# Performance work log

Measured on AMD Instinct MI355X. Metric: run time of the kernel, lower is better.

## Reference

```python
import jax, jax.numpy as jnp
import numpy as np

B, P, T = 32, 196, 32           # batch, num pixels (14*14), seq_len
E, H, A, V = 512, 512, 256, 30000  # embed, hidden, attention, vocab
FEAT = 2048

def _ln(x, g, b, eps=1e-5):
    m = jnp.mean(x, -1, keepdims=True)
    v = jnp.mean((x - m) ** 2, -1, keepdims=True)
    return (x - m) / jnp.sqrt(v + eps) * g + b

def setup_inputs() -> dict:
    key = jax.random.key(0)
    ks = iter(jax.random.split(key, 32))
    def rn(shape, s=0.05):
        return (jax.random.normal(next(ks), shape, dtype=jnp.float32) * s)
    inp = {
        'features': jax.random.normal(next(ks), (B, P, FEAT), dtype=jnp.float32),
        'captions': jax.random.randint(next(ks), (B, T), 0, V),
        # feature adapter Linear(2048->E) + LayerNorm
        'Wad': rn((E, FEAT)), 'bad': jnp.zeros((E,), jnp.float32),
        'g_ad': jnp.ones((E,), jnp.float32), 'b_ad': jnp.zeros((E,), jnp.float32),
        # additive attention
        'We': rn((A, E)), 'be': jnp.zeros((A,), jnp.float32),
        'Wd': rn((A, H)), 'bd': jnp.zeros((A,), jnp.float32),
        'Wf': rn((1, A)), 'bf': jnp.zeros((1,), jnp.float32),
        # embedding table (uniform(-0.1,0.1) as in torch init)
        'emb': jax.random.uniform(next(ks), (V, E), jnp.float32, -0.1, 0.1),
        # LSTM layer 0: input 2E, layer 1: input H; gates order i,f,g,o; forget bias 1
        'W_ih0': rn((4 * H, 2 * E)), 'W_hh0': rn((4 * H, H)),
        'b_ih0': jnp.concatenate([jnp.zeros(H), jnp.ones(H), jnp.zeros(2 * H)]).astype(jnp.float32),
        'b_hh0': jnp.zeros((4 * H,), jnp.float32),
        'W_ih1': rn((4 * H, H)), 'W_hh1': rn((4 * H, H)),
        'b_ih1': jnp.concatenate([jnp.zeros(H), jnp.ones(H), jnp.zeros(2 * H)]).astype(jnp.float32),
        'b_hh1': jnp.zeros((4 * H,), jnp.float32),
        # output head
        'W1': rn((H // 2, H)), 'b1': jnp.zeros((H // 2,), jnp.float32),
        'g1': jnp.ones((H // 2,), jnp.float32), 'bb1': jnp.zeros((H // 2,), jnp.float32),
        'W2': rn((V, H // 2)), 'b2': jnp.zeros((V,), jnp.float32),
    }
    return inp

def reference(features, captions, Wad, bad, g_ad, b_ad, We, be, Wd, bd, Wf, bf,
              emb, W_ih0, W_hh0, b_ih0, b_hh0, W_ih1, W_hh1, b_ih1, b_hh1,
              W1, b1, g1, bb1, W2, b2):
    # feature adapter (dropout = identity in eval)
    enc = _ln(jax.nn.relu(features @ Wad.T + bad), g_ad, b_ad)   # [B,P,E]
    att1 = enc @ We.T + be                                        # [B,P,A] (same every step)
    embs = emb[captions]                                          # [B,T,E]

    def lstm_cell(x, h, c, Wih, Whh, bih, bhh):
        gates = x @ Wih.T + bih + h @ Whh.T + bhh                 # [B,4H]
        i, f, g, o = jnp.split(gates, 4, axis=1)
        c_n = jax.nn.sigmoid(f) * c + jax.nn.sigmoid(i) * jnp.tanh(g)
        h_n = jax.nn.sigmoid(o) * jnp.tanh(c_n)
        return h_n, c_n

    def step(carry, emb_t):
        h, c = carry                                              # each [2,B,H]
        # additive attention against top-layer hidden state
        att2 = h[1] @ Wd.T + bd                                   # [B,A]
        e = (jax.nn.relu(att1 + att2[:, None, :]) @ Wf.T + bf)[..., 0]  # [B,P]
        alpha = jax.nn.softmax(e, axis=1)                         # (max-subtract is folded in)
        ctx = jnp.einsum('bp,bpe->be', alpha, enc)                # [B,E]
        x = jnp.concatenate([emb_t, ctx], axis=1)                 # [B,2E]
        h0, c0 = lstm_cell(x,  h[0], c[0], W_ih0, W_hh0, b_ih0, b_hh0)
        h1, c1 = lstm_cell(h0, h[1], c[1], W_ih1, W_hh1, b_ih1, b_hh1)
        out = jax.nn.relu(_ln(h1 @ W1.T + b1, g1, bb1))
        out = jnp.clip(out @ W2.T + b2, -10.0, 10.0)              # [B,V]
        return (jnp.stack([h0, h1]), jnp.stack([c0, c1])), out

    h0 = jnp.zeros((2, B, H), jnp.float32)
    c0 = jnp.zeros((2, B, H), jnp.float32)
    _, outs = jax.lax.scan(step, (h0, c0), jnp.swapaxes(embs, 0, 1))
    return jnp.swapaxes(outs, 0, 1)                               # [B,T,V]
```

## Files before the change

kernel.cpp:

```cpp
#include <hip/hip_runtime.h>

#define B_ 32
#define P_ 196
#define T_ 32
#define E_ 512
#define H_ 512
#define A_ 256
#define V_ 30000
#define FEAT_ 2048

typedef unsigned short u16;
typedef __attribute__((ext_vector_type(8))) short bf16x8;
typedef __attribute__((ext_vector_type(4))) float fx4;

#define MFMA16 __builtin_amdgcn_mfma_f32_16x16x32_bf16

__device__ __forceinline__ u16 f2b(float f){
  unsigned u = __builtin_bit_cast(unsigned, f);
  u += 0x7FFFu + ((u >> 16) & 1u);
  return (u16)(u >> 16);
}
__device__ __forceinline__ float b2f(u16 h){
  unsigned u = ((unsigned)h) << 16;
  return __builtin_bit_cast(float, u);
}
__device__ __forceinline__ float sigm(float x){ return 1.f/(1.f + __expf(-x)); }

__global__ void k_convert(const float* __restrict__ src, u16* __restrict__ dst, int n8){
  int i = blockIdx.x*256 + threadIdx.x;
  if (i >= n8) return;
  const float4* s = (const float4*)src + (size_t)i*2;
  float4 a = s[0], b = s[1];
  ushort4* d = (ushort4*)dst + (size_t)i*2;
  d[0] = make_ushort4(f2b(a.x), f2b(a.y), f2b(a.z), f2b(a.w));
  d[1] = make_ushort4(f2b(b.x), f2b(b.y), f2b(b.z), f2b(b.w));
}

__global__ void k_gather(const float* __restrict__ emb, const int* __restrict__ cap,
                         u16* __restrict__ dst){
  int r = blockIdx.x, l = threadIdx.x;
  int t = r >> 5, b = r & 31;
  int c = cap[b*T_ + t];
  const float4* s = (const float4*)(emb + (size_t)c*E_) + l*2;
  float4 a = s[0], bb = s[1];
  ushort4* d = (ushort4*)(dst + (size_t)r*E_) + l*2;
  d[0] = make_ushort4(f2b(a.x), f2b(a.y), f2b(a.z), f2b(a.w));
  d[1] = make_ushort4(f2b(bb.x), f2b(bb.y), f2b(bb.z), f2b(bb.w));
}

__global__ void k_pack_wd2(const float* __restrict__ Wd, unsigned* __restrict__ dst){
  int i = blockIdx.x*256 + threadIdx.x;
  if (i >= 256*256) return;
  int n = i & 255, kp = i >> 8;
  unsigned lo = f2b(Wd[n*512 + 2*kp]);
  unsigned hi = f2b(Wd[n*512 + 2*kp + 1]);
  dst[i] = lo | (hi << 16);
}

__global__ void k_pack_g0(const float* __restrict__ Wih, const float* __restrict__ Whh,
                          u16* __restrict__ dst){
  int eid = blockIdx.x*256 + threadIdx.x;
  if (eid >= 6144*512) return;
  int j = eid & 7, l = (eid >> 3) & 63, frag = eid >> 9;
  int ks = frag % 12; int rest = frag / 12;
  int kw = rest & 3, q = (rest >> 2) & 3, s = rest >> 4;
  int n = q*512 + s*16 + (l & 15);
  int k = kw*384 + ks*32 + ((l >> 4) << 3) + j;
  float v = (k < 1024) ? Wih[(size_t)n*1024 + k] : Whh[(size_t)n*512 + (k - 1024)];
  dst[eid] = f2b(v);
}

__global__ void k_pack_w1p(const float* __restrict__ Wih, const float* __restrict__ Whh,
                           u16* __restrict__ dst){
  int eid = blockIdx.x*256 + threadIdx.x;
  if (eid >= 32*128*512) return;
  int j = eid & 7, l = (eid >> 3) & 63, f = eid >> 9;
  int nf = f & 127, s = f >> 7;
  int np = nf*16 + (l & 15);
  int k = ((l >> 4) << 3) + j;
  int orig = ((np >> 4) & 3)*512 + (np >> 6)*16 + (np & 15);
  float v = (k < 16) ? Wih[(size_t)orig*512 + s*16 + k]
                     : Whh[(size_t)orig*512 + s*16 + (k - 16)];
  dst[eid] = f2b(v);
}

__global__ void k_bias_pack(const float* __restrict__ bih, const float* __restrict__ bhh,
                            float* __restrict__ dst){
  int n = blockIdx.x*256 + threadIdx.x;
  if (n >= 2048) return;
  int c = n & 15, q = (n >> 4) & 3, s = n >> 6;
  int orig = q*512 + s*16 + c;
  dst[n] = bih[orig] + bhh[orig];
}

template<int MODE, int BM, int BN>
__launch_bounds__(256)
__global__ void k_gemm(const u16* __restrict__ A, const u16* __restrict__ W,
                       const float* __restrict__ bias, float* __restrict__ outF,
                       u16* __restrict__ outB, int M, int N, int K){
  constexpr int NI = BN/32, MI = BM/32;
  __shared__ __align__(16) u16 As[BM][40];
  __shared__ __align__(16) u16 Bs[BN][40];
  int tid = threadIdx.x;
  int l = tid & 63, w = tid >> 6;
  int wr = w >> 1, wc = w & 1;
  int m0 = blockIdx.y * BM, n0 = blockIdx.x * BN;
  fx4 acc[MI][NI];
  #pragma unroll
  for (int i=0;i<MI;i++)
    #pragma unroll
    for (int j=0;j<NI;j++) acc[i][j] = (fx4){0.f,0.f,0.f,0.f};
  int r = tid >> 2, seg = tid & 3;
  int lr = l & 15, lg = l >> 4;
  for (int k0 = 0; k0 < K; k0 += 32){
    #pragma unroll
    for (int pa=0; pa<BM/64; pa++)
      *(uint4*)&As[r+pa*64][seg*8] = *(const uint4*)(A + (size_t)(m0+r+pa*64)*K + k0 + seg*8);
    uint4 z = {0u,0u,0u,0u};
    #pragma unroll
    for (int pb=0; pb<BN/64; pb++){
      int rb = n0 + r + pb*64;
      *(uint4*)&Bs[r+pb*64][seg*8] = (rb < N) ? *(const uint4*)(W + (size_t)rb*K + k0 + seg*8) : z;
    }
    __syncthreads();
    bf16x8 av[MI], bv[NI];
    #pragma unroll
    for (int mi=0; mi<MI; mi++) av[mi] = *(const bf16x8*)&As[wr*(BM/2) + mi*16 + lr][lg*8];
    #pragma unroll
    for (int ni=0; ni<NI; ni++) bv[ni] = *(const bf16x8*)&Bs[wc*(BN/2) + ni*16 + lr][lg*8];
    #pragma unroll
    for (int mi=0; mi<MI; mi++)
      #pragma unroll
      for (int ni=0; ni<NI; ni++)
        acc[mi][ni] = MFMA16(av[mi], bv[ni], acc[mi][ni], 0, 0, 0);
    __syncthreads();
  }
  #pragma unroll
  for (int mi=0; mi<MI; mi++)
    #pragma unroll
    for (int ni=0; ni<NI; ni++){
      int col = n0 + wc*(BN/2) + ni*16 + lr;
      if (col >= N) continue;
      float bvs = bias[col];
      #pragma unroll
      for (int reg=0; reg<4; reg++){
        int rowm = m0 + wr*(BM/2) + mi*16 + lg*4 + reg;
        float v = acc[mi][ni][reg] + bvs;
        if (MODE == 0){ v = fmaxf(v, 0.f); outB[(size_t)rowm*N + col] = f2b(v); }
        else if (MODE == 1){ outB[(size_t)rowm*N + col] = f2b(v); }
        else if (MODE == 2){ outF[(size_t)rowm*N + col] = v; }
        else {
          v = fminf(fmaxf(v, -10.f), 10.f);
          outF[(size_t)rowm*V_ + col] = v;
        }
      }
    }
}

__global__ void k_ln1(const u16* __restrict__ pre, const float* __restrict__ g,
                      const float* __restrict__ bt, u16* __restrict__ enc){
  int row = blockIdx.x; int l = threadIdx.x;
  bf16x8 vv = *(const bf16x8*)(pre + (size_t)row*E_ + l*8);
  float x[8]; float s = 0.f;
  #pragma unroll
  for (int i=0;i<8;i++){ x[i] = b2f((u16)vv[i]); s += x[i]; }
  #pragma unroll
  for (int off=32; off; off>>=1) s += __shfl_xor(s, off, 64);
  float mean = s * (1.f/512.f);
  float vs = 0.f;
  #pragma unroll
  for (int i=0;i<8;i++){ float d = x[i]-mean; vs += d*d; }
  #pragma unroll
  for (int off=32; off; off>>=1) vs += __shfl_xor(vs, off, 64);
  float inv = rsqrtf(vs*(1.f/512.f) + 1e-5f);
  int c0 = l*8;
  u16 o[8];
  #pragma unroll
  for (int i=0;i<8;i++) o[i] = f2b((x[i]-mean)*inv*g[c0+i] + bt[c0+i]);
  ushort4* d = (ushort4*)(enc + (size_t)row*E_ + c0);
  d[0] = make_ushort4(o[0],o[1],o[2],o[3]);
  d[1] = make_ushort4(o[4],o[5],o[6],o[7]);
}

__global__ void k_ln2(const float* __restrict__ pre1, const float* __restrict__ g,
                      const float* __restrict__ bb, u16* __restrict__ hid){
  int row = blockIdx.x; int l = threadIdx.x;
  float4 v = *(const float4*)(pre1 + (size_t)row*256 + l*4);
  float x[4] = {v.x, v.y, v.z, v.w};
  float s = x[0]+x[1]+x[2]+x[3];
  #pragma unroll
  for (int off=32; off; off>>=1) s += __shfl_xor(s, off, 64);
  float mean = s * (1.f/256.f);
  float vs = 0.f;
  #pragma unroll
  for (int i=0;i<4;i++){ float d = x[i]-mean; vs += d*d; }
  #pragma unroll
  for (int off=32; off; off>>=1) vs += __shfl_xor(vs, off, 64);
  float inv = rsqrtf(vs*(1.f/256.f) + 1e-5f);
  int c0 = l*4;
  u16 o[4];
  #pragma unroll
  for (int i=0;i<4;i++) o[i] = f2b(fmaxf((x[i]-mean)*inv*g[c0+i] + bb[c0+i], 0.f));
  *(ushort4*)(hid + (size_t)row*256 + c0) = make_ushort4(o[0],o[1],o[2],o[3]);
}

__launch_bounds__(1024)
__global__ void k_ly(const float* __restrict__ part1, const float* __restrict__ bias1p,
                     float* __restrict__ c1buf, u16* __restrict__ h1all,
                     const unsigned* __restrict__ Wd2, const float* __restrict__ bd,
                     const u16* __restrict__ att1b, const u16* __restrict__ enc16,
                     const float* __restrict__ Wf, const float* __restrict__ bfp,
                     const u16* __restrict__ embs, u16* __restrict__ xh0cur, int t){
  int b = blockIdx.x, tid = threadIdx.x;
  int l = tid & 63, wid = tid >> 6;
  __shared__ float g1s[2048];
  __shared__ float h1s[512];
  __shared__ float a2p[4][256];
  __shared__ float a2[256], ev[256], red[8], wfv[256], bdv[256];
  __shared__ float cb[4][256][2];
  if (tid < 256){ wfv[tid] = Wf[tid]; bdv[tid] = bd[tid]; }
  float bf0 = bfp[0];

  if (t > 0){
    float acc0 = bias1p[tid], acc1 = bias1p[tid + 1024];
    #pragma unroll 4
    for (int s2=0; s2<32; ++s2){
      const float* pp = part1 + ((size_t)(s2*32 + b))*2048;
      acc0 += pp[tid];
      acc1 += pp[tid + 1024];
    }
    g1s[tid] = acc0; g1s[tid + 1024] = acc1;
    __syncthreads();
    if (tid < 512){
      int h = tid, s4 = h >> 4, c = h & 15, base = s4*64 + c;
      float gi = g1s[base], gf = g1s[base+16], gg = g1s[base+32], go = g1s[base+48];
      float cold = c1buf[b*512 + h];
      float cn = sigm(gf)*cold + sigm(gi)*tanhf(gg);
      c1buf[b*512 + h] = cn;
      float hn = sigm(go)*tanhf(cn);
      h1s[h] = hn;
      h1all[((size_t)b*T_ + (t-1))*512 + h] = f2b(hn);
    }
  } else {
    if (tid < 512) h1s[tid] = 0.f;
  }
  __syncthreads();
  if (t >= T_) return;

  {
    int n = tid & 255, kq = tid >> 8;
    float acc = 0.f;
    const unsigned* wp = Wd2 + (size_t)kq*64*256 + n;
    #pragma unroll 8
    for (int kp2 = 0; kp2 < 64; ++kp2){
      unsigned wv = wp[(size_t)kp2*256];
      int k0 = (kq*64 + kp2)*2;
      acc += h1s[k0]   * b2f((u16)(wv & 0xFFFFu))
           + h1s[k0+1] * b2f((u16)(wv >> 16));
    }
    a2p[kq][n] = acc;
  }
  __syncthreads();
  if (tid < 256) a2[tid] = a2p[0][tid] + a2p[1][tid] + a2p[2][tid] + a2p[3][tid] + bdv[tid];
  __syncthreads();
  for (int pi = 0; pi < 13; ++pi){
    int p = pi*16 + wid;
    if (p < P_){
      ushort4 av4 = *(const ushort4*)(att1b + (size_t)(b*P_ + p)*A_ + l*4);
      int j0 = l*4;
      float sum = fmaxf(b2f(av4.x)+a2[j0],  0.f)*wfv[j0]
                + fmaxf(b2f(av4.y)+a2[j0+1],0.f)*wfv[j0+1]
                + fmaxf(b2f(av4.z)+a2[j0+2],0.f)*wfv[j0+2]
                + fmaxf(b2f(av4.w)+a2[j0+3],0.f)*wfv[j0+3];
      #pragma unroll
      for (int off=32; off; off>>=1) sum += __shfl_xor(sum, off, 64);
      if (l == 0) ev[p] = sum + bf0;
    }
  }
  __syncthreads();
  if (tid < 256){
    float v = (tid < P_) ? ev[tid] : -1e30f;
    float m = v;
    #pragma unroll
    for (int off=32; off; off>>=1) m = fmaxf(m, __shfl_xor(m, off, 64));
    if (l == 0) red[wid] = m;
  }
  __syncthreads();
  float mg = fmaxf(fmaxf(red[0],red[1]), fmaxf(red[2],red[3]));
  if (tid < 256){
    float ex = (tid < P_) ? __expf(ev[tid] - mg) : 0.f;
    float ss = ex;
    #pragma unroll
    for (int off=32; off; off>>=1) ss += __shfl_xor(ss, off, 64);
    if (l == 0) red[4+wid] = ss;
    ev[tid] = ex;
  }
  __syncthreads();
  float inv = 1.f/(red[4]+red[5]+red[6]+red[7]);
  {
    int j = tid & 255, pq = tid >> 8;
    float A0 = 0.f, A1 = 0.f;
    const unsigned* ep = (const unsigned*)enc16 + ((size_t)b*P_ + pq*49)*256 + j;
    #pragma unroll 7
    for (int pi = 0; pi < 49; ++pi){
      unsigned vv = ep[(size_t)pi*256];
      float al = ev[pq*49 + pi];
      A0 += al * b2f((u16)(vv & 0xFFFFu));
      A1 += al * b2f((u16)(vv >> 16));
    }
    cb[pq][j][0] = A0; cb[pq][j][1] = A1;
  }
  __syncthreads();
  if (tid < 256){
    float c0 = (cb[0][tid][0]+cb[1][tid][0]+cb[2][tid][0]+cb[3][tid][0]) * inv;
    float c1 = (cb[0][tid][1]+cb[1][tid][1]+cb[2][tid][1]+cb[3][tid][1]) * inv;
    unsigned o = (unsigned)f2b(c0) | (((unsigned)f2b(c1)) << 16);
    *((unsigned*)(xh0cur + (size_t)b*1536 + 512) + tid) = o;
    ((unsigned*)(xh0cur + (size_t)b*1536))[tid] =
        ((const unsigned*)(embs + (size_t)(t*32+b)*E_))[tid];
  }
}

__launch_bounds__(1024)
__global__ void k_lx(const u16* __restrict__ xh0cur, u16* __restrict__ xh0nxt,
                     const u16* __restrict__ Wg0pk, const float* __restrict__ bias0p,
                     const u16* __restrict__ W1ppk, const u16* __restrict__ h1all,
                     float* __restrict__ c0buf, float* __restrict__ part1, int t){
  __shared__ float part[16][32][16];
  __shared__ float gsum[4][32][16];
  __shared__ __align__(16) u16 As[32][40];
  int tid = threadIdx.x, s = blockIdx.x;
  int l = tid & 63, kw = tid >> 6, lr = l & 15, lg = l >> 4;

  bf16x8 a[2][3];
  #pragma unroll
  for (int mi=0;mi<2;mi++)
    #pragma unroll
    for (int ks=0;ks<3;ks++)
      a[mi][ks] = *(const bf16x8*)(xh0cur + (size_t)(mi*16+lr)*1536 + kw*96 + ks*32 + lg*8);
  for (int q=0;q<4;q++){
    fx4 acc0 = (fx4){0,0,0,0}, acc1 = (fx4){0,0,0,0};
    const u16* wp = Wg0pk + (size_t)(((s*4+q)*4 + (kw>>2))*12 + (kw&3)*3)*512 + l*8;
    #pragma unroll
    for (int ks=0;ks<3;ks++){
      bf16x8 bf8 = *(const bf16x8*)(wp + ks*512);
      acc0 = MFMA16(a[0][ks], bf8, acc0, 0,0,0);
      acc1 = MFMA16(a[1][ks], bf8, acc1, 0,0,0);
    }
    #pragma unroll
    for (int reg=0;reg<4;reg++){
      part[kw][lg*4+reg][lr]    = acc0[reg];
      part[kw][16+lg*4+reg][lr] = acc1[reg];
    }
    __syncthreads();
    if (tid < 512){
      int bb = tid >> 4, c = tid & 15;
      float g = bias0p[s*64 + q*16 + c];
      #pragma unroll
      for (int kw2=0; kw2<16; ++kw2) g += part[kw2][bb][c];
      gsum[q][bb][c] = g;
    }
    __syncthreads();
  }
  if (tid < 256){
    int bb = tid >> 3, kk = (tid & 7)*2;
    unsigned hv = 0;
    if (t > 0) hv = *(const unsigned*)(h1all + ((size_t)bb*T_ + (t-1))*512 + s*16 + kk);
    *(unsigned*)&As[bb][16+kk] = hv;
  }
  if (tid < 512){
    int bb = tid >> 4, c = tid & 15;
    int h = s*16 + c;
    float gi = gsum[0][bb][c], gf = gsum[1][bb][c], gg = gsum[2][bb][c], go = gsum[3][bb][c];
    float cold = c0buf[bb*512 + h];
    float cn = sigm(gf)*cold + sigm(gi)*tanhf(gg);
    c0buf[bb*512 + h] = cn;
    u16 hb = f2b(sigm(go)*tanhf(cn));
    xh0nxt[(size_t)bb*1536 + 1024 + h] = hb;
    As[bb][c] = hb;
  }
  __syncthreads();
  bf16x8 pa0 = *(const bf16x8*)&As[lr][lg*8];
  bf16x8 pa1 = *(const bf16x8*)&As[16+lr][lg*8];
  #pragma unroll 2
  for (int i=0;i<8;i++){
    int nf = kw*8 + i;
    bf16x8 bf8 = *(const bf16x8*)(W1ppk + (size_t)(s*128 + nf)*512 + l*8);
    fx4 A0 = MFMA16(pa0, bf8, (fx4){0,0,0,0}, 0,0,0);
    fx4 A1 = MFMA16(pa1, bf8, (fx4){0,0,0,0}, 0,0,0);
    float* o = part1 + ((size_t)s*32)*2048 + nf*16 + lr;
    #pragma unroll
    for (int reg=0;reg<4;reg++){
      o[(size_t)(lg*4+reg)*2048]    = A0[reg];
      o[(size_t)(16+lg*4+reg)*2048] = A1[reg];
    }
  }
}

extern "C" void kernel_launch(void* const* d_in, const int* in_sizes, int n_in,
                              void* d_out, int out_size, void* d_ws, size_t ws_size,
                              hipStream_t stream){
  (void)in_sizes; (void)n_in; (void)out_size; (void)ws_size;
  const float* features = (const float*)d_in[0];
  const int*   captions = (const int*)d_in[1];
  const float* Wad  = (const float*)d_in[2];
  const float* bad  = (const float*)d_in[3];
  const float* g_ad = (const float*)d_in[4];
  const float* b_ad = (const float*)d_in[5];
  const float* We   = (const float*)d_in[6];
  const float* be   = (const float*)d_in[7];
  const float* Wd   = (const float*)d_in[8];
  const float* bd   = (const float*)d_in[9];
  const float* Wf   = (const float*)d_in[10];
  const float* bfp  = (const float*)d_in[11];
  const float* emb  = (const float*)d_in[12];
  const float* W_ih0 = (const float*)d_in[13];
  const float* W_hh0 = (const float*)d_in[14];
  const float* b_ih0 = (const float*)d_in[15];
  const float* b_hh0 = (const float*)d_in[16];
  const float* W_ih1 = (const float*)d_in[17];
  const float* W_hh1 = (const float*)d_in[18];
  const float* b_ih1 = (const float*)d_in[19];
  const float* b_hh1 = (const float*)d_in[20];
  const float* W1  = (const float*)d_in[21];
  const float* b1  = (const float*)d_in[22];
  const float* g1  = (const float*)d_in[23];
  const float* bb1 = (const float*)d_in[24];
  const float* W2  = (const float*)d_in[25];
  const float* b2  = (const float*)d_in[26];
  float* out = (float*)d_out;

  char* wsb = (char*)d_ws;
  size_t off = 0;
  auto alloc = [&](size_t bytes)->char*{
    char* p = wsb + off; off += (bytes + 255) & ~(size_t)255; return p;
  };
  u16* fb16    = (u16*)alloc((size_t)6272*2048*2);
  u16* Wad16   = (u16*)alloc((size_t)512*2048*2);
  u16* We16    = (u16*)alloc((size_t)256*512*2);
  u16* W1_16   = (u16*)alloc((size_t)256*512*2);
  u16* W2_16   = (u16*)alloc((size_t)30000*256*2);
  unsigned* Wd2 = (unsigned*)alloc((size_t)256*256*4);
  u16* Wg0pk   = (u16*)alloc((size_t)2048*1536*2);
  u16* W1ppk   = (u16*)alloc((size_t)32*128*512*2);
  float* bias0p = (float*)alloc(2048*4);
  float* bias1p = (float*)alloc(2048*4);
  u16* embs16  = (u16*)alloc((size_t)1024*512*2);
  u16* pre16   = (u16*)alloc((size_t)6272*512*2);
  u16* enc16   = (u16*)alloc((size_t)6272*512*2);
  u16* att1_16 = (u16*)alloc((size_t)6272*256*2);
  u16* xh0     = (u16*)alloc((size_t)2*32*1536*2);
  float* c0buf = (float*)alloc(32*512*4);
  float* c1buf = (float*)alloc(32*512*4);
  float* part1 = (float*)alloc((size_t)32*32*2048*4);
  u16* h1all16 = (u16*)alloc((size_t)1024*512*2);
  float* pre1  = (float*)alloc((size_t)1024*256*4);
  u16* hid16   = (u16*)alloc((size_t)1024*256*2);

  auto cdiv = [](int a, int b){ return (a+b-1)/b; };

  hipMemsetAsync(xh0, 0, 196608 + 65536 + 65536, stream);

  k_convert<<<cdiv(6272*2048/8,256),256,0,stream>>>(features, fb16, 6272*2048/8);
  k_convert<<<cdiv(512*2048/8,256),256,0,stream>>>(Wad, Wad16, 512*2048/8);
  k_convert<<<cdiv(256*512/8,256),256,0,stream>>>(We, We16, 256*512/8);
  k_convert<<<cdiv(256*512/8,256),256,0,stream>>>(W1, W1_16, 256*512/8);
  k_convert<<<cdiv(30000*256/8,256),256,0,stream>>>(W2, W2_16, 30000*256/8);
  k_pack_wd2<<<cdiv(256*256,256),256,0,stream>>>(Wd, Wd2);
  k_pack_g0<<<cdiv(6144*512,256),256,0,stream>>>(W_ih0, W_hh0, Wg0pk);
  k_pack_w1p<<<cdiv(32*128*512,256),256,0,stream>>>(W_ih1, W_hh1, W1ppk);
  k_bias_pack<<<8,256,0,stream>>>(b_ih0, b_hh0, bias0p);
  k_bias_pack<<<8,256,0,stream>>>(b_ih1, b_hh1, bias1p);
  k_gather<<<1024,64,0,stream>>>(emb, captions, embs16);

  k_gemm<0,64,64><<<dim3(8,98),256,0,stream>>>(fb16, Wad16, bad, nullptr, pre16, 6272, 512, 2048);
  k_ln1<<<6272,64,0,stream>>>(pre16, g_ad, b_ad, enc16);
  k_gemm<1,64,64><<<dim3(4,98),256,0,stream>>>(enc16, We16, be, nullptr, att1_16, 6272, 256, 512);

  u16* xb[2] = { xh0, xh0 + 32*1536 };
  for (int t = 0; t < T_; ++t){
    k_ly<<<32,1024,0,stream>>>(part1, bias1p, c1buf, h1all16, Wd2, bd,
                               att1_16, enc16, Wf, bfp, embs16, xb[t&1], t);
    k_lx<<<32,1024,0,stream>>>(xb[t&1], xb[1-(t&1)], Wg0pk, bias0p,
                               W1ppk, h1all16, c0buf, part1, t);
  }
  k_ly<<<32,1024,0,stream>>>(part1, bias1p, c1buf, h1all16, Wd2, bd,
                             att1_16, enc16, Wf, bfp, embs16, xb[0], T_);

  k_gemm<2,64,64><<<dim3(4,16),256,0,stream>>>(h1all16, W1_16, b1, pre1, nullptr, 1024, 256, 512);
  k_ln2<<<1024,64,0,stream>>>(pre1, g1, bb1, hid16);
  k_gemm<3,64,128><<<dim3(235,16),256,0,stream>>>(hid16, W2_16, b2, out, nullptr, 1024, 30000, 256);
}
```

Before: 1.395 ms.

## Overlap output head and W2 conversion with recurrent steps on idle CUs

The recurrent kernels only use 32 blocks, leaving most CUs idle. Extra blocks are added to each step launch. For the first steps they convert W2 to bf16, and afterwards they compute the W1+LayerNorm projection and the vocab head for the previous timestep. This hides the large head GEMM behind the serial recurrence and removes the separate tail GEMMs. The cost is more blocks per launch, a larger shared footprint, and finer-grained head tiles that reload W2 every step.

New measurement: 1.653 ms. +18.5%, slower.

```diff
diff --git a/kernel.cpp b/kernel.cpp
--- a/kernel.cpp
+++ b/kernel.cpp
@@ -25,6 +25,17 @@
   return __builtin_bit_cast(float, u);
 }
 __device__ __forceinline__ float sigm(float x){ return 1.f/(1.f + __expf(-x)); }
+
+struct RecLyS {
+  float g1s[2048]; float h1s[512]; float a2p[4][256];
+  float a2[256]; float ev[256]; float red[8]; float wfv[256]; float bdv[256];
+  float cb[4][256][2];
+};
+struct RecLxS {
+  float part[16][32][16]; float gsum[4][32][16]; u16 As[32][40];
+};
+struct HeadS { u16 hA[32][264]; u16 hB[256][40]; };
+struct W1S   { float red2[1024]; float mv[64]; };
 
 __global__ void k_convert(const float* __restrict__ src, u16* __restrict__ dst, int n8){
   int i = blockIdx.x*256 + threadIdx.x;
@@ -96,8 +107,8 @@
 template<int MODE, int BM, int BN>
 __launch_bounds__(256)
 __global__ void k_gemm(const u16* __restrict__ A, const u16* __restrict__ W,
-                       const float* __restrict__ bias, float* __restrict__ outF,
-                       u16* __restrict__ outB, int M, int N, int K){
+                       const float* __restrict__ bias, u16* __restrict__ outB,
+                       int M, int N, int K){
   constexpr int NI = BN/32, MI = BM/32;
   __shared__ __align__(16) u16 As[BM][40];
   __shared__ __align__(16) u16 Bs[BN][40];
@@ -146,13 +157,8 @@
       for (int reg=0; reg<4; reg++){
         int rowm = m0 + wr*(BM/2) + mi*16 + lg*4 + reg;
         float v = acc[mi][ni][reg] + bvs;
-        if (MODE == 0){ v = fmaxf(v, 0.f); outB[(size_t)rowm*N + col] = f2b(v); }
-        else if (MODE == 1){ outB[(size_t)rowm*N + col] = f2b(v); }
-        else if (MODE == 2){ outF[(size_t)rowm*N + col] = v; }
-        else {
-          v = fminf(fmaxf(v, -10.f), 10.f);
-          outF[(size_t)rowm*V_ + col] = v;
-        }
+        if (MODE == 0) v = fmaxf(v, 0.f);
+        outB[(size_t)rowm*N + col] = f2b(v);
       }
     }
 }
@@ -182,26 +188,115 @@
   d[1] = make_ushort4(o[4],o[5],o[6],o[7]);
 }
 
-__global__ void k_ln2(const float* __restrict__ pre1, const float* __restrict__ g,
-                      const float* __restrict__ bb, u16* __restrict__ hid){
-  int row = blockIdx.x; int l = threadIdx.x;
-  float4 v = *(const float4*)(pre1 + (size_t)row*256 + l*4);
-  float x[4] = {v.x, v.y, v.z, v.w};
-  float s = x[0]+x[1]+x[2]+x[3];
-  #pragma unroll
-  for (int off=32; off; off>>=1) s += __shfl_xor(s, off, 64);
-  float mean = s * (1.f/256.f);
-  float vs = 0.f;
-  #pragma unroll
-  for (int i=0;i<4;i++){ float d = x[i]-mean; vs += d*d; }
-  #pragma unroll
-  for (int off=32; off; off>>=1) vs += __shfl_xor(vs, off, 64);
-  float inv = rsqrtf(vs*(1.f/256.f) + 1e-5f);
-  int c0 = l*4;
-  u16 o[4];
-  #pragma unroll
-  for (int i=0;i<4;i++) o[i] = f2b(fmaxf((x[i]-mean)*inv*g[c0+i] + bb[c0+i], 0.f));
-  *(ushort4*)(hid + (size_t)row*256 + c0) = make_ushort4(o[0],o[1],o[2],o[3]);
+__device__ __forceinline__ void w2cvt_chunk(const float* __restrict__ W2f,
+                                            u16* __restrict__ W2b, int cw, int tid){
+  int i = cw*1024 + tid;
+  if (i >= (V_*A_)/8) return;
+  const float4* s = (const float4*)W2f + (size_t)i*2;
+  float4 a = s[0], b = s[1];
+  ushort4* d = (ushort4*)W2b + (size_t)i*2;
+  d[0] = make_ushort4(f2b(a.x), f2b(a.y), f2b(a.z), f2b(a.w));
+  d[1] = make_ushort4(f2b(b.x), f2b(b.y), f2b(b.z), f2b(b.w));
+}
+
+__device__ __forceinline__ void w1ln_block(const u16* __restrict__ h1all,
+    const u16* __restrict__ W1, const float* __restrict__ b1,
+    const float* __restrict__ g1v, const float* __restrict__ bb1,
+    u16* __restrict__ hid, int u, int tid, float* red2, float* mv){
+  int l = tid & 63, w = tid >> 6, lr = l & 15, lg = l >> 4;
+  fx4 acc[2] = {{0,0,0,0},{0,0,0,0}};
+  for (int k0 = 0; k0 < 512; k0 += 32){
+    bf16x8 bv  = *(const bf16x8*)(W1 + (size_t)(w*16+lr)*512 + k0 + lg*8);
+    bf16x8 av0 = *(const bf16x8*)(h1all + ((size_t)lr*T_ + u)*512 + k0 + lg*8);
+    bf16x8 av1 = *(const bf16x8*)(h1all + ((size_t)(16+lr)*T_ + u)*512 + k0 + lg*8);
+    acc[0] = MFMA16(av0, bv, acc[0], 0,0,0);
+    acc[1] = MFMA16(av1, bv, acc[1], 0,0,0);
+  }
+  int col = w*16 + lr;
+  float bc = b1[col];
+  float val[2][4], s1[2][4], s2[2][4];
+  #pragma unroll
+  for (int mi=0;mi<2;mi++)
+    #pragma unroll
+    for (int reg=0;reg<4;reg++){
+      float v = acc[mi][reg] + bc;
+      val[mi][reg] = v; s1[mi][reg] = v; s2[mi][reg] = v*v;
+    }
+  #pragma unroll
+  for (int off=1; off<16; off<<=1){
+    #pragma unroll
+    for (int mi=0;mi<2;mi++)
+      #pragma unroll
+      for (int reg=0;reg<4;reg++){
+        s1[mi][reg] += __shfl_xor(s1[mi][reg], off, 64);
+        s2[mi][reg] += __shfl_xor(s2[mi][reg], off, 64);
+      }
+  }
+  if (lr == 0){
+    #pragma unroll
+    for (int mi=0;mi<2;mi++)
+      #pragma unroll
+      for (int reg=0;reg<4;reg++){
+        int row = mi*16 + lg*4 + reg;
+        red2[(0*16 + w)*32 + row] = s1[mi][reg];
+        red2[(16   + w)*32 + row] = s2[mi][reg];
+      }
+  }
+  __syncthreads();
+  if (tid < 64){
+    int which = tid >> 5, row = tid & 31;
+    float s = 0.f;
+    #pragma unroll
+    for (int ww=0; ww<16; ++ww) s += red2[(which*16 + ww)*32 + row];
+    mv[which*32 + row] = s;
+  }
+  __syncthreads();
+  #pragma unroll
+  for (int mi=0;mi<2;mi++)
+    #pragma unroll
+    for (int reg=0;reg<4;reg++){
+      int row = mi*16 + lg*4 + reg;
+      float mean = mv[row] * (1.f/256.f);
+      float var  = mv[32+row] * (1.f/256.f) - mean*mean;
+      float inv  = rsqrtf(var + 1e-5f);
+      float o = fmaxf((val[mi][reg]-mean)*inv*g1v[col] + bb1[col], 0.f);
+      hid[((size_t)u*32 + row)*256 + col] = f2b(o);
+    }
+}
+
+__device__ __forceinline__ void head_chunk(const u16* __restrict__ hid,
+    const u16* __restrict__ W2, const float* __restrict__ b2,
+    float* __restrict__ out, int u, int c, int tid,
+    u16 (*hA)[264], u16 (*hB)[40]){
+  if (c >= 118) return;
+  int l = tid & 63, w = tid >> 6, lr = l & 15, lg = l >> 4;
+  int v0 = c*256;
+  { int arow = tid >> 5, ak = (tid & 31)*8;
+    *(uint4*)&hA[arow][ak] = *(const uint4*)(hid + ((size_t)u*32 + arow)*256 + ak); }
+  fx4 acc0 = {0,0,0,0}, acc1 = {0,0,0,0};
+  int r = tid >> 2, seg = tid & 3;
+  for (int k0 = 0; k0 < 256; k0 += 32){
+    uint4 z = {0u,0u,0u,0u};
+    int rb = v0 + r;
+    *(uint4*)&hB[r][seg*8] = (rb < V_) ? *(const uint4*)(W2 + (size_t)rb*256 + k0 + seg*8) : z;
+    __syncthreads();
+    bf16x8 bv  = *(const bf16x8*)&hB[w*16 + lr][lg*8];
+    bf16x8 av0 = *(const bf16x8*)&hA[lr][k0 + lg*8];
+    bf16x8 av1 = *(const bf16x8*)&hA[16 + lr][k0 + lg*8];
+    acc0 = MFMA16(av0, bv, acc0, 0,0,0);
+    acc1 = MFMA16(av1, bv, acc1, 0,0,0);
+    __syncthreads();
+  }
+  int col = v0 + w*16 + lr;
+  if (col < V_){
+    float bb = b2[col];
+    #pragma unroll
+    for (int reg=0; reg<4; reg++){
+      int r0 = lg*4 + reg, r1 = 16 + lg*4 + reg;
+      out[((size_t)r0*T_ + u)*V_ + col] = fminf(fmaxf(acc0[reg]+bb, -10.f), 10.f);
+      out[((size_t)r1*T_ + u)*V_ + col] = fminf(fmaxf(acc1[reg]+bb, -10.f), 10.f);
+    }
+  }
 }
 
 __launch_bounds__(1024)
@@ -210,15 +305,27 @@
                      const unsigned* __restrict__ Wd2, const float* __restrict__ bd,
                      const u16* __restrict__ att1b, const u16* __restrict__ enc16,
                      const float* __restrict__ Wf, const float* __restrict__ bfp,
-                     const u16* __restrict__ embs, u16* __restrict__ xh0cur, int t){
-  int b = blockIdx.x, tid = threadIdx.x;
+                     const u16* __restrict__ embs, u16* __restrict__ xh0cur, int t,
+                     int auxmode, int auxp,
+                     const float* __restrict__ W2f, u16* __restrict__ W2b,
+                     const u16* __restrict__ hid16, const float* __restrict__ b2,
+                     float* __restrict__ out){
+  constexpr unsigned SB = sizeof(RecLyS) > sizeof(HeadS) ? sizeof(RecLyS) : sizeof(HeadS);
+  __shared__ __align__(16) char shbuf[SB];
+  int bid = blockIdx.x, tid = threadIdx.x;
+  if (bid >= 32){
+    int a = bid - 32;
+    if (auxmode == 1) w2cvt_chunk(W2f, W2b, auxp + a, tid);
+    else {
+      HeadS& HS = *(HeadS*)shbuf;
+      head_chunk(hid16, W2b, b2, out, auxp, a, tid, HS.hA, HS.hB);
+    }
+    return;
+  }
+  RecLyS& S = *(RecLyS*)shbuf;
+  int b = bid;
   int l = tid & 63, wid = tid >> 6;
-  __shared__ float g1s[2048];
-  __shared__ float h1s[512];
-  __shared__ float a2p[4][256];
-  __shared__ float a2[256], ev[256], red[8], wfv[256], bdv[256];
-  __shared__ float cb[4][256][2];
-  if (tid < 256){ wfv[tid] = Wf[tid]; bdv[tid] = bd[tid]; }
+  if (tid < 256){ S.wfv[tid] = Wf[tid]; S.bdv[tid] = bd[tid]; }
   float bf0 = bfp[0];
 
   if (t > 0){
@@ -229,20 +336,20 @@
       acc0 += pp[tid];
       acc1 += pp[tid + 1024];
     }
-    g1s[tid] = acc0; g1s[tid + 1024] = acc1;
+    S.g1s[tid] = acc0; S.g1s[tid + 1024] = acc1;
     __syncthreads();
     if (tid < 512){
       int h = tid, s4 = h >> 4, c = h & 15, base = s4*64 + c;
-      float gi = g1s[base], gf = g1s[base+16], gg = g1s[base+32], go = g1s[base+48];
+      float gi = S.g1s[base], gf = S.g1s[base+16], gg = S.g1s[base+32], go = S.g1s[base+48];
       float cold = c1buf[b*512 + h];
       float cn = sigm(gf)*cold + sigm(gi)*tanhf(gg);
       c1buf[b*512 + h] = cn;
       float hn = sigm(go)*tanhf(cn);
-      h1s[h] = hn;
+      S.h1s[h] = hn;
       h1all[((size_t)b*T_ + (t-1))*512 + h] = f2b(hn);
     }
   } else {
-    if (tid < 512) h1s[tid] = 0.f;
+    if (tid < 512) S.h1s[tid] = 0.f;
   }
   __syncthreads();
   if (t >= T_) return;
@@ -255,48 +362,48 @@
     for (int kp2 = 0; kp2 < 64; ++kp2){
       unsigned wv = wp[(size_t)kp2*256];
       int k0 = (kq*64 + kp2)*2;
-      acc += h1s[k0]   * b2f((u16)(wv & 0xFFFFu))
-           + h1s[k0+1] * b2f((u16)(wv >> 16));
-    }
-    a2p[kq][n] = acc;
-  }
-  __syncthreads();
-  if (tid < 256) a2[tid] = a2p[0][tid] + a2p[1][tid] + a2p[2][tid] + a2p[3][tid] + bdv[tid];
+      acc += S.h1s[k0]   * b2f((u16)(wv & 0xFFFFu))
+           + S.h1s[k0+1] * b2f((u16)(wv >> 16));
+    }
+    S.a2p[kq][n] = acc;
+  }
+  __syncthreads();
+  if (tid < 256) S.a2[tid] = S.a2p[0][tid] + S.a2p[1][tid] + S.a2p[2][tid] + S.a2p[3][tid] + S.bdv[tid];
   __syncthreads();
   for (int pi = 0; pi < 13; ++pi){
     int p = pi*16 + wid;
     if (p < P_){
       ushort4 av4 = *(const ushort4*)(att1b + (size_t)(b*P_ + p)*A_ + l*4);
       int j0 = l*4;
-      float sum = fmaxf(b2f(av4.x)+a2[j0],  0.f)*wfv[j0]
-                + fmaxf(b2f(av4.y)+a2[j0+1],0.f)*wfv[j0+1]
-                + fmaxf(b2f(av4.z)+a2[j0+2],0.f)*wfv[j0+2]
-                + fmaxf(b2f(av4.w)+a2[j0+3],0.f)*wfv[j0+3];
+      float sum = fmaxf(b2f(av4.x)+S.a2[j0],  0.f)*S.wfv[j0]
+                + fmaxf(b2f(av4.y)+S.a2[j0+1],0.f)*S.wfv[j0+1]
+                + fmaxf(b2f(av4.z)+S.a2[j0+2],0.f)*S.wfv[j0+2]
+                + fmaxf(b2f(av4.w)+S.a2[j0+3],0.f)*S.wfv[j0+3];
       #pragma unroll
       for (int off=32; off; off>>=1) sum += __shfl_xor(sum, off, 64);
-      if (l == 0) ev[p] = sum + bf0;
+      if (l == 0) S.ev[p] = sum + bf0;
     }
   }
   __syncthreads();
   if (tid < 256){
-    float v = (tid < P_) ? ev[tid] : -1e30f;
+    float v = (tid < P_) ? S.ev[tid] : -1e30f;
     float m = v;
     #pragma unroll
     for (int off=32; off; off>>=1) m = fmaxf(m, __shfl_xor(m, off, 64));
-    if (l == 0) red[wid] = m;
-  }
-  __syncthreads();
-  float mg = fmaxf(fmaxf(red[0],red[1]), fmaxf(red[2],red[3]));
+    if (l == 0) S.red[wid] = m;
+  }
+  __syncthreads();
+  float mg = fmaxf(fmaxf(S.red[0],S.red[1]), fmaxf(S.red[2],S.red[3]));
   if (tid < 256){
-    float ex = (tid < P_) ? __expf(ev[tid] - mg) : 0.f;
+    float ex = (tid < P_) ? __expf(S.ev[tid] - mg) : 0.f;
     float ss = ex;
     #pragma unroll
     for (int off=32; off; off>>=1) ss += __shfl_xor(ss, off, 64);
-    if (l == 0) red[4+wid] = ss;
-    ev[tid] = ex;
-  }
-  __syncthreads();
-  float inv = 1.f/(red[4]+red[5]+red[6]+red[7]);
+    if (l == 0) S.red[4+wid] = ss;
+    S.ev[tid] = ex;
+  }
+  __syncthreads();
+  float inv = 1.f/(S.red[4]+S.red[5]+S.red[6]+S.red[7]);
   {
     int j = tid & 255, pq = tid >> 8;
     float A0 = 0.f, A1 = 0.f;
@@ -304,16 +411,16 @@
     #pragma unroll 7
     for (int pi = 0; pi < 49; ++pi){
       unsigned vv = ep[(size_t)pi*256];
-      float al = ev[pq*49 + pi];
+      float al = S.ev[pq*49 + pi];
       A0 += al * b2f((u16)(vv & 0xFFFFu));
       A1 += al * b2f((u16)(vv >> 16));
     }
-    cb[pq][j][0] = A0; cb[pq][j][1] = A1;
+    S.cb[pq][j][0] = A0; S.cb[pq][j][1] = A1;
   }
   __syncthreads();
   if (tid < 256){
-    float c0 = (cb[0][tid][0]+cb[1][tid][0]+cb[2][tid][0]+cb[3][tid][0]) * inv;
-    float c1 = (cb[0][tid][1]+cb[1][tid][1]+cb[2][tid][1]+cb[3][tid][1]) * inv;
+    float c0 = (S.cb[0][tid][0]+S.cb[1][tid][0]+S.cb[2][tid][0]+S.cb[3][tid][0]) * inv;
+    float c1 = (S.cb[0][tid][1]+S.cb[1][tid][1]+S.cb[2][tid][1]+S.cb[3][tid][1]) * inv;
     unsigned o = (unsigned)f2b(c0) | (((unsigned)f2b(c1)) << 16);
     *((unsigned*)(xh0cur + (size_t)b*1536 + 512) + tid) = o;
     ((unsigned*)(xh0cur + (size_t)b*1536))[tid] =
@@ -325,11 +432,35 @@
 __global__ void k_lx(const u16* __restrict__ xh0cur, u16* __restrict__ xh0nxt,
                      const u16* __restrict__ Wg0pk, const float* __restrict__ bias0p,
                      const u16* __restrict__ W1ppk, const u16* __restrict__ h1all,
-                     float* __restrict__ c0buf, float* __restrict__ part1, int t){
-  __shared__ float part[16][32][16];
-  __shared__ float gsum[4][32][16];
-  __shared__ __align__(16) u16 As[32][40];
-  int tid = threadIdx.x, s = blockIdx.x;
+                     float* __restrict__ c0buf, float* __restrict__ part1, int t,
+                     int auxmode, int auxp,
+                     const float* __restrict__ W2f, u16* __restrict__ W2b,
+                     u16* __restrict__ hid16, const float* __restrict__ b2,
+                     float* __restrict__ out,
+                     const u16* __restrict__ W1_16, const float* __restrict__ b1,
+                     const float* __restrict__ g1v, const float* __restrict__ bb1){
+  constexpr unsigned SA = sizeof(RecLxS) > sizeof(HeadS) ? sizeof(RecLxS) : sizeof(HeadS);
+  constexpr unsigned SB = SA > sizeof(W1S) ? SA : sizeof(W1S);
+  __shared__ __align__(16) char shbuf[SB];
+  int bid = blockIdx.x, tid = threadIdx.x;
+  if (bid == 32){
+    if (t >= 1){
+      W1S& WS = *(W1S*)shbuf;
+      w1ln_block(h1all, W1_16, b1, g1v, bb1, hid16, t-1, tid, WS.red2, WS.mv);
+    }
+    return;
+  }
+  if (bid > 32){
+    int a = bid - 33;
+    if (auxmode == 1) w2cvt_chunk(W2f, W2b, auxp + a, tid);
+    else {
+      HeadS& HS = *(HeadS*)shbuf;
+      head_chunk(hid16, W2b, b2, out, auxp, 59 + a, tid, HS.hA, HS.hB);
+    }
+    return;
+  }
+  RecLxS& S = *(RecLxS*)shbuf;
+  int s = bid;
   int l = tid & 63, kw = tid >> 6, lr = l & 15, lg = l >> 4;
 
   bf16x8 a[2][3];
@@ -349,16 +480,16 @@
     }
     #pragma unroll
     for (int reg=0;reg<4;reg++){
-      part[kw][lg*4+reg][lr]    = acc0[reg];
-      part[kw][16+lg*4+reg][lr] = acc1[reg];
+      S.part[kw][lg*4+reg][lr]    = acc0[reg];
+      S.part[kw][16+lg*4+reg][lr] = acc1[reg];
     }
     __syncthreads();
     if (tid < 512){
       int bb = tid >> 4, c = tid & 15;
       float g = bias0p[s*64 + q*16 + c];
       #pragma unroll
-      for (int kw2=0; kw2<16; ++kw2) g += part[kw2][bb][c];
-      gsum[q][bb][c] = g;
+      for (int kw2=0; kw2<16; ++kw2) g += S.part[kw2][bb][c];
+      S.gsum[q][bb][c] = g;
     }
     __syncthreads();
   }
@@ -366,22 +497,22 @@
     int bb = tid >> 3, kk = (tid & 7)*2;
     unsigned hv = 0;
     if (t > 0) hv = *(const unsigned*)(h1all + ((size_t)bb*T_ + (t-1))*512 + s*16 + kk);
-    *(unsigned*)&As[bb][16+kk] = hv;
+    *(unsigned*)&S.As[bb][16+kk] = hv;
   }
   if (tid < 512){
     int bb = tid >> 4, c = tid & 15;
     int h = s*16 + c;
-    float gi = gsum[0][bb][c], gf = gsum[1][bb][c], gg = gsum[2][bb][c], go = gsum[3][bb][c];
+    float gi = S.gsum[0][bb][c], gf = S.gsum[1][bb][c], gg = S.gsum[2][bb][c], go = S.gsum[3][bb][c];
     float cold = c0buf[bb*512 + h];
     float cn = sigm(gf)*cold + sigm(gi)*tanhf(gg);
     c0buf[bb*512 + h] = cn;
     u16 hb = f2b(sigm(go)*tanhf(cn));
     xh0nxt[(size_t)bb*1536 + 1024 + h] = hb;
-    As[bb][c] = hb;
-  }
-  __syncthreads();
-  bf16x8 pa0 = *(const bf16x8*)&As[lr][lg*8];
-  bf16x8 pa1 = *(const bf16x8*)&As[16+lr][lg*8];
+    S.As[bb][c] = hb;
+  }
+  __syncthreads();
+  bf16x8 pa0 = *(const bf16x8*)&S.As[lr][lg*8];
+  bf16x8 pa1 = *(const bf16x8*)&S.As[16+lr][lg*8];
   #pragma unroll 2
   for (int i=0;i<8;i++){
     int nf = kw*8 + i;
@@ -395,6 +526,25 @@
       o[(size_t)(16+lg*4+reg)*2048] = A1[reg];
     }
   }
+}
+
+__launch_bounds__(1024)
+__global__ void k_aux(int w1t, int u, int cofs,
+                      const u16* __restrict__ h1all, const u16* __restrict__ W1_16,
+                      const float* __restrict__ b1, const float* __restrict__ g1v,
+                      const float* __restrict__ bb1, u16* __restrict__ hid16,
+                      const u16* __restrict__ W2b, const float* __restrict__ b2,
+                      float* __restrict__ out){
+  constexpr unsigned SB = sizeof(HeadS) > sizeof(W1S) ? sizeof(HeadS) : sizeof(W1S);
+  __shared__ __align__(16) char shbuf[SB];
+  int bid = blockIdx.x, tid = threadIdx.x;
+  if (bid == 0 && w1t >= 0){
+    W1S& WS = *(W1S*)shbuf;
+    w1ln_block(h1all, W1_16, b1, g1v, bb1, hid16, w1t, tid, WS.red2, WS.mv);
+    return;
+  }
+  HeadS& HS = *(HeadS*)shbuf;
+  head_chunk(hid16, W2b, b2, out, u, cofs + bid, tid, HS.hA, HS.hB);
 }
 
 extern "C" void kernel_launch(void* const* d_in, const int* in_sizes, int n_in,
@@ -454,7 +604,6 @@
   float* c1buf = (float*)alloc(32*512*4);
   float* part1 = (float*)alloc((size_t)32*32*2048*4);
   u16* h1all16 = (u16*)alloc((size_t)1024*512*2);
-  float* pre1  = (float*)alloc((size_t)1024*256*4);
   u16* hid16   = (u16*)alloc((size_t)1024*256*2);
 
   auto cdiv = [](int a, int b){ return (a+b-1)/b; };
@@ -465,7 +614,6 @@
   k_convert<<<cdiv(512*2048/8,256),256,0,stream>>>(Wad, Wad16, 512*2048/8);
   k_convert<<<cdiv(256*512/8,256),256,0,stream>>>(We, We16, 256*512/8);
   k_convert<<<cdiv(256*512/8,256),256,0,stream>>>(W1, W1_16, 256*512/8);
-  k_convert<<<cdiv(30000*256/8,256),256,0,stream>>>(W2, W2_16, 30000*256/8);
   k_pack_wd2<<<cdiv(256*256,256),256,0,stream>>>(Wd, Wd2);
   k_pack_g0<<<cdiv(6144*512,256),256,0,stream>>>(W_ih0, W_hh0, Wg0pk);
   k_pack_w1p<<<cdiv(32*128*512,256),256,0,stream>>>(W_ih1, W_hh1, W1ppk);
@@ -473,21 +621,31 @@
   k_bias_pack<<<8,256,0,stream>>>(b_ih1, b_hh1, bias1p);
   k_gather<<<1024,64,0,stream>>>(emb, captions, embs16);
 
-  k_gemm<0,64,64><<<dim3(8,98),256,0,stream>>>(fb16, Wad16, bad, nullptr, pre16, 6272, 512, 2048);
+  k_gemm<0,64,64><<<dim3(8,98),256,0,stream>>>(fb16, Wad16, bad, pre16, 6272, 512, 2048);
   k_ln1<<<6272,64,0,stream>>>(pre16, g_ad, b_ad, enc16);
-  k_gemm<1,64,64><<<dim3(4,98),256,0,stream>>>(enc16, We16, be, nullptr, att1_16, 6272, 256, 512);
+  k_gemm<1,64,64><<<dim3(4,98),256,0,stream>>>(enc16, We16, be, att1_16, 6272, 256, 512);
 
   u16* xb[2] = { xh0, xh0 + 32*1536 };
   for (int t = 0; t < T_; ++t){
-    k_ly<<<32,1024,0,stream>>>(part1, bias1p, c1buf, h1all16, Wd2, bd,
-                               att1_16, enc16, Wf, bfp, embs16, xb[t&1], t);
-    k_lx<<<32,1024,0,stream>>>(xb[t&1], xb[1-(t&1)], Wg0pk, bias0p,
-                               W1ppk, h1all16, c0buf, part1, t);
-  }
-  k_ly<<<32,1024,0,stream>>>(part1, bias1p, c1buf, h1all16, Wd2, bd,
-                             att1_16, enc16, Wf, bfp, embs16, xb[0], T_);
-
-  k_gemm<2,64,64><<<dim3(4,16),256,0,stream>>>(h1all16, W1_16, b1, pre1, nullptr, 1024, 256, 512);
-  k_ln2<<<1024,64,0,stream>>>(pre1, g1, bb1, hid16);
-  k_gemm<3,64,128><<<dim3(235,16),256,0,stream>>>(hid16, W2_16, b2, out, nullptr, 1024, 30000, 256);
-}
+    int am   = (t < 3) ? 1 : 2;
+    int lyp  = (t < 3) ? t*314       : (t-3);
+    int lxp  = (t < 3) ? t*314 + 157 : (t-3);
+    int naux = (t < 3) ? 157 : 59;
+    k_ly<<<32+naux,1024,0,stream>>>(part1, bias1p, c1buf, h1all16, Wd2, bd,
+                                    att1_16, enc16, Wf, bfp, embs16, xb[t&1], t,
+                                    am, lyp, W2, W2_16, hid16, b2, out);
+    k_lx<<<33+naux,1024,0,stream>>>(xb[t&1], xb[1-(t&1)], Wg0pk, bias0p,
+                                    W1ppk, h1all16, c0buf, part1, t,
+                                    am, lxp, W2, W2_16, hid16, b2, out,
+                                    W1_16, b1, g1, bb1);
+  }
+  k_ly<<<91,1024,0,stream>>>(part1, bias1p, c1buf, h1all16, Wd2, bd,
+                             att1_16, enc16, Wf, bfp, embs16, xb[0], T_,
+                             2, 29, W2, W2_16, hid16, b2, out);
+  k_aux<<<60,1024,0,stream>>>(31, 29, 58, h1all16, W1_16, b1, g1, bb1,
+                              hid16, W2_16, b2, out);
+  k_aux<<<118,1024,0,stream>>>(-1, 30, 0, h1all16, W1_16, b1, g1, bb1,
+                               hid16, W2_16, b2, out);
+  k_aux<<<118,1024,0,stream>>>(-1, 31, 0, h1all16, W1_16, b1, g1, bb1,
+                               hid16, W2_16, b2, out);
+}
```
